# Optimization experiments

Measured on AMD Instinct MI355X. Metric: run time of the kernel, lower is better.

Reference implementation:

```python
import jax, jax.numpy as jnp
import numpy as np


def setup_inputs() -> dict:
    key = jax.random.key(0)
    k1, k2 = jax.random.split(key)
    x = jax.random.normal(k1, (128, 25, 512), dtype=jnp.float32)
    high = jax.random.normal(k2, (64, 20, 512), dtype=jnp.float32)  # (C, n, d)
    return {"x": x, "high": high}


def reference(x, high):
    # x: (b, res, d); high: (C, n, d) learned per-class support basis
    b, res, d = x.shape
    C, n, _ = high.shape
    q = x.reshape(b * res, d)                     # (Q, d)
    lam = n / d                                   # ridge coefficient = n/d
    ct = jnp.swapaxes(high, 1, 2)                 # (C, d, n)
    cct = high @ ct                               # (C, n, n) small Gram matrices
    inv = jnp.linalg.inv(cct + lam * jnp.eye(n, dtype=x.dtype))  # (C, n, n)
    ctinv = ct @ inv @ high                       # (C, d, d) per-class projector
    # reconstruct each query through each class projector: (C, Q, d)
    t = jnp.einsum('qd,cde->cqe', q, ctinv)
    dist = jnp.sum((t - q[None, :, :]) ** 2, axis=2).T  # (Q, C)
    logits = -dist.reshape(b, res, C).mean(axis=1)       # (b, C)
    # min-max scaler per row
    mn = logits.min(axis=1, keepdims=True)
    mx = logits.max(axis=1, keepdims=True)
    return (logits - mn) / (mx - mn)
```

## Files before the change

kernel.cpp:

```cpp
#include <hip/hip_runtime.h>

typedef __bf16 v8bf __attribute__((ext_vector_type(8)));
typedef float  v4f  __attribute__((ext_vector_type(4)));

#define D     512
#define NSUP  20
#define NC    64
#define RES   25
#define BB    128
#define LAM   (20.0f/512.0f)
#define KT    32
#define NKT   (D/KT)
#define CPB   8
#define COLS  160
#define NFRAG 10
#define MFRAG 4
#define LRSZ  820

__device__ __forceinline__ ushort bf_hi(float v) {
    uint32_t b = __float_as_uint(v);
    return (ushort)((b + 0x7FFF + ((b >> 16) & 1)) >> 16);
}
__device__ __forceinline__ float us2f(ushort u) {
    return __uint_as_float(((uint32_t)u) << 16);
}

__global__ __launch_bounds__(256) void k_prep1(const float* __restrict__ high,
                                               float* __restrict__ LR) {
    const int cls = blockIdx.x;
    const int t   = threadIdx.x;
    __shared__ float Hc[NSUP * 516];
    __shared__ float Gs[NSUP * NSUP];

    for (int i = t; i < NSUP * (D / 4); i += 256) {
        int r = i >> 7, c4 = (i & 127) << 2;
        *(float4*)&Hc[r * 516 + c4] = *(const float4*)&high[(cls * NSUP + r) * D + c4];
    }
    __syncthreads();

    for (int e = t; e < NSUP * NSUP; e += 256) {
        int i = e / NSUP, j = e % NSUP;
        if (i <= j) {
            float s = 0.f;
            for (int k = 0; k < D; k += 4) {
                float4 a = *(float4*)&Hc[i * 516 + k];
                float4 b = *(float4*)&Hc[j * 516 + k];
                s += a.x * b.x + a.y * b.y + a.z * b.z + a.w * b.w;
            }
            Gs[i * NSUP + j] = s;
            Gs[j * NSUP + i] = s;
        }
    }
    __syncthreads();

    if (t < 64) {
        const int c  = t & 31;
        const int gp = t >> 5;
        const float dlam = gp ? 2.0f * LAM : LAM;
        float m[NSUP];
        if (c < NSUP) {
            #pragma unroll
            for (int i = 0; i < NSUP; ++i) m[i] = Gs[i * NSUP + c];
            #pragma unroll
            for (int i = 0; i < NSUP; ++i) if (i == c) m[i] += dlam;
        }
        #pragma unroll
        for (int k = 0; k < NSUP; ++k) {
            float piv = __shfl(m[k], k, 32);
            float sq  = sqrtf(piv);
            float rsq = 1.0f / sq;
            float lck = m[k] * rsq;
            if (c == k) {
                m[k] = sq;
                #pragma unroll
                for (int i = k + 1; i < NSUP; ++i) m[i] *= rsq;
            }
            #pragma unroll
            for (int i = k + 1; i < NSUP; ++i) {
                float lik = __shfl(m[i], k, 32);
                if (c > k) m[i] -= lik * lck;
            }
        }
        if (c < NSUP) {
            float* base = LR + cls * LRSZ + (gp ? 400 : 0);
            #pragma unroll
            for (int i = 0; i < NSUP; ++i) if (i >= c) base[i * NSUP + c] = m[i];
            if (!gp) LR[cls * LRSZ + 800 + c] = 1.0f / m[c];
        }
    }
}

__global__ __launch_bounds__(256) void k_prep2(const float* __restrict__ high,
                                               const float* __restrict__ LR,
                                               ushort* __restrict__ Hth,
                                               ushort* __restrict__ Htl) {
    const int cls = blockIdx.x;
    const int col = blockIdx.y * 256 + threadIdx.x;
    const int t   = threadIdx.x;
    __shared__ float Ls[400], Rs[400], rL[NSUP];

    for (int i = t; i < 400; i += 256) Ls[i] = LR[cls * LRSZ + i];
    for (int i = t; i < 400; i += 256) Rs[i] = LR[cls * LRSZ + 400 + i];
    if (t < NSUP) rL[t] = LR[cls * LRSZ + 800 + t];
    __syncthreads();

    float h[NSUP];
    #pragma unroll
    for (int m = 0; m < NSUP; ++m) h[m] = high[(cls * NSUP + m) * D + col];
    #pragma unroll
    for (int i = 0; i < NSUP; ++i) {
        float s = h[i];
        #pragma unroll
        for (int m = 0; m < i; ++m) s -= Ls[i * NSUP + m] * h[m];
        h[i] = s * rL[i];
    }
    #pragma unroll
    for (int i = NSUP - 1; i >= 0; --i) {
        float s = h[i];
        #pragma unroll
        for (int m = i + 1; m < NSUP; ++m) s -= Ls[m * NSUP + i] * h[m];
        h[i] = s * rL[i];
    }
    #pragma unroll
    for (int i = 0; i < NSUP; ++i) {
        float s = 0.f;
        #pragma unroll
        for (int m = i; m < NSUP; ++m) s += Rs[m * NSUP + i] * h[m];
        ushort hh = bf_hi(s);
        float  rr = s - us2f(hh);
        Hth[(cls * NSUP + i) * D + col] = hh;
        Htl[(cls * NSUP + i) * D + col] = bf_hi(rr);
    }
}

__global__ __launch_bounds__(256, 2) void k_main(const float* __restrict__ x,
                                                 const ushort* __restrict__ Hth,
                                                 const ushort* __restrict__ Htl,
                                                 float* __restrict__ S) {
    const int cg = blockIdx.x, bp = blockIdx.y;
    const int t = threadIdx.x, lane = t & 63, wid = t >> 6;
    const int wm = wid >> 1, wn = wid & 1;

    __shared__ __align__(16) ushort XH[2][MFRAG * 512];
    __shared__ __align__(16) ushort XL[2][MFRAG * 512];
    __shared__ __align__(16) ushort HH[2][NFRAG * 512];
    __shared__ __align__(16) ushort HL[2][NFRAG * 512];
    __shared__ float colsum[2][COLS];

    v4f acc[2][5];
    #pragma unroll
    for (int a = 0; a < 2; ++a)
        #pragma unroll
        for (int b = 0; b < 5; ++b) acc[a][b] = (v4f){0.f, 0.f, 0.f, 0.f};

    auto stageX = [&](int buf, int kt) {
        #pragma unroll
        for (int s2 = 0; s2 < 2; ++s2) {
            int g = t + 256 * s2;
            int p = g >> 3;
            int k0 = (g & 7) << 2;
            float4 v = make_float4(0.f, 0.f, 0.f, 0.f);
            int r = p & 31;
            if (r < RES)
                v = *(const float4*)&x[(((bp << 1) + (p >> 5)) * RES + r) * D + kt + k0];
            ushort4 hu, lu;
            {
                ushort h; float rr;
                h = bf_hi(v.x); rr = v.x - us2f(h); hu.x = h; lu.x = bf_hi(rr);
                h = bf_hi(v.y); rr = v.y - us2f(h); hu.y = h; lu.y = bf_hi(rr);
                h = bf_hi(v.z); rr = v.z - us2f(h); hu.z = h; lu.z = bf_hi(rr);
                h = bf_hi(v.w); rr = v.w - us2f(h); hu.w = h; lu.w = bf_hi(rr);
            }
            int m = p >> 4, i = p & 15, q = k0 >> 3, off = (k0 & 7);
            int base = m * 512 + (q * 16 + i) * 8 + off;
            *(ushort4*)&XH[buf][base] = hu;
            *(ushort4*)&XL[buf][base] = lu;
        }
    };

    auto stageH = [&](int buf, int kt) {
        #pragma unroll
        for (int j = 0; j < 5; ++j) {
            int cid = wid * 5 + j;
            int n = (cid < 10) ? cid : cid - 10;
            const ushort* src = (cid < 10) ? Hth : Htl;
            ushort* dst = (cid < 10) ? &HH[buf][n * 512] : &HL[buf][n * 512];
            int row = cg * COLS + n * 16 + (lane & 15);
            const ushort* gp = &src[row * D + kt + ((lane >> 4) << 3)];
            __builtin_amdgcn_global_load_lds(
                (const __attribute__((address_space(1))) void*)gp,
                (__attribute__((address_space(3))) void*)dst, 16, 0, 0);
        }
    };

    auto compute = [&](int buf) {
        v8bf ah[2], al[2];
        #pragma unroll
        for (int mf = 0; mf < 2; ++mf) {
            int f = wm * 2 + mf;
            ah[mf] = *(const v8bf*)&XH[buf][f * 512 + lane * 8];
            al[mf] = *(const v8bf*)&XL[buf][f * 512 + lane * 8];
        }
        #pragma unroll
        for (int nf = 0; nf < 5; ++nf) {
            int f = wn * 5 + nf;
            v8bf bh = *(const v8bf*)&HH[buf][f * 512 + lane * 8];
            v8bf bl = *(const v8bf*)&HL[buf][f * 512 + lane * 8];
            #pragma unroll
            for (int mf = 0; mf < 2; ++mf) {
                acc[mf][nf] = __builtin_amdgcn_mfma_f32_16x16x32_bf16(ah[mf], bh, acc[mf][nf], 0, 0, 0);
                acc[mf][nf] = __builtin_amdgcn_mfma_f32_16x16x32_bf16(ah[mf], bl, acc[mf][nf], 0, 0, 0);
                acc[mf][nf] = __builtin_amdgcn_mfma_f32_16x16x32_bf16(al[mf], bh, acc[mf][nf], 0, 0, 0);
            }
        }
    };

    stageX(0, 0);
    stageH(0, 0);
    __syncthreads();
    for (int step = 0; step < NKT; ++step) {
        int cur = step & 1;
        if (step + 1 < NKT) {
            stageH(cur ^ 1, (step + 1) * KT);
            stageX(cur ^ 1, (step + 1) * KT);
        }
        compute(cur);
        __syncthreads();
    }

    #pragma unroll
    for (int nf = 0; nf < 5; ++nf) {
        float part = 0.f;
        #pragma unroll
        for (int mf = 0; mf < 2; ++mf)
            #pragma unroll
            for (int j = 0; j < 4; ++j) part += acc[mf][nf][j] * acc[mf][nf][j];
        part += __shfl_xor(part, 16);
        part += __shfl_xor(part, 32);
        if ((lane >> 4) == 0) colsum[wm][wn * 80 + nf * 16 + lane] = part;
    }
    __syncthreads();
    if (t < 16) {
        int b = t >> 3, c = t & 7;
        float s = 0.f;
        #pragma unroll
        for (int i = 0; i < NSUP; ++i) s += colsum[b][c * 20 + i];
        S[((bp << 1) + b) * NC + cg * CPB + c] = s;
    }
}

__global__ __launch_bounds__(64) void k_minmax(const float* __restrict__ S,
                                               float* __restrict__ out) {
    const int b    = blockIdx.x;
    const int lane = threadIdx.x;
    float s  = S[b * NC + lane];
    float mn = s, mx = s;
    #pragma unroll
    for (int off = 32; off > 0; off >>= 1) {
        mn = fminf(mn, __shfl_xor(mn, off, 64));
        mx = fmaxf(mx, __shfl_xor(mx, off, 64));
    }
    out[b * NC + lane] = (s - mn) / (mx - mn);
}

extern "C" void kernel_launch(void* const* d_in, const int* in_sizes, int n_in,
                              void* d_out, int out_size, void* d_ws, size_t ws_size,
                              hipStream_t stream) {
    const float* x    = (const float*)d_in[0];
    const float* high = (const float*)d_in[1];
    float* out = (float*)d_out;

    ushort* Hth = (ushort*)d_ws;
    ushort* Htl = Hth + NC * NSUP * D;
    float*  S   = (float*)(Htl + NC * NSUP * D);
    float*  LR  = S + BB * NC;

    k_prep1 <<<NC, 256, 0, stream>>>(high, LR);
    k_prep2 <<<dim3(NC, 2), 256, 0, stream>>>(high, LR, Hth, Htl);
    k_main  <<<dim3(CPB, BB / 2), 256, 0, stream>>>(x, Hth, Htl, S);
    k_minmax<<<BB, 64, 0, stream>>>(S, out);
}
```

Before: 110.9 us.

## Fuse prep kernels and fold min-max normalization into main kernel via tickets

Merges the two preparation kernels into one, so each block computes the Cholesky factors in shared memory and applies them directly instead of round-tripping through global memory. Each of the two blocks per class recomputes the Gram and factorization redundantly. The final min-max kernel is removed: the last main-kernel block for each batch pair, found with an atomic ticket counter, normalizes the rows. This cuts two kernel launches and adds atomics and fences.

```diff
diff --git a/kernel.cpp b/kernel.cpp
--- a/kernel.cpp
+++ b/kernel.cpp
@@ -15,7 +15,6 @@
 #define COLS  160
 #define NFRAG 10
 #define MFRAG 4
-#define LRSZ  820
 
 __device__ __forceinline__ ushort bf_hi(float v) {
     uint32_t b = __float_as_uint(v);
@@ -25,12 +24,18 @@
     return __uint_as_float(((uint32_t)u) << 16);
 }
 
-__global__ __launch_bounds__(256) void k_prep1(const float* __restrict__ high,
-                                               float* __restrict__ LR) {
-    const int cls = blockIdx.x;
-    const int t   = threadIdx.x;
+__global__ __launch_bounds__(256) void k_prep(const float* __restrict__ high,
+                                              ushort* __restrict__ Hth,
+                                              ushort* __restrict__ Htl,
+                                              int* __restrict__ ticket) {
+    const int cls  = blockIdx.x;
+    const int half = blockIdx.y;
+    const int t    = threadIdx.x;
     __shared__ float Hc[NSUP * 516];
     __shared__ float Gs[NSUP * NSUP];
+    __shared__ float Ls[400], Rs[400], rL[NSUP];
+
+    if (cls == 0 && half == 0 && t < NC) ticket[t] = 0;
 
     for (int i = t; i < NSUP * (D / 4); i += 256) {
         int r = i >> 7, c4 = (i & 127) << 2;
@@ -82,31 +87,18 @@
             }
         }
         if (c < NSUP) {
-            float* base = LR + cls * LRSZ + (gp ? 400 : 0);
-            #pragma unroll
-            for (int i = 0; i < NSUP; ++i) if (i >= c) base[i * NSUP + c] = m[i];
-            if (!gp) LR[cls * LRSZ + 800 + c] = 1.0f / m[c];
-        }
-    }
-}
-
-__global__ __launch_bounds__(256) void k_prep2(const float* __restrict__ high,
-                                               const float* __restrict__ LR,
-                                               ushort* __restrict__ Hth,
-                                               ushort* __restrict__ Htl) {
-    const int cls = blockIdx.x;
-    const int col = blockIdx.y * 256 + threadIdx.x;
-    const int t   = threadIdx.x;
-    __shared__ float Ls[400], Rs[400], rL[NSUP];
-
-    for (int i = t; i < 400; i += 256) Ls[i] = LR[cls * LRSZ + i];
-    for (int i = t; i < 400; i += 256) Rs[i] = LR[cls * LRSZ + 400 + i];
-    if (t < NSUP) rL[t] = LR[cls * LRSZ + 800 + t];
-    __syncthreads();
-
+            float* Lout = gp ? Rs : Ls;
+            #pragma unroll
+            for (int i = 0; i < NSUP; ++i) if (i >= c) Lout[i * NSUP + c] = m[i];
+            if (!gp) rL[c] = 1.0f / m[c];
+        }
+    }
+    __syncthreads();
+
+    const int col = half * 256 + t;
     float h[NSUP];
     #pragma unroll
-    for (int m = 0; m < NSUP; ++m) h[m] = high[(cls * NSUP + m) * D + col];
+    for (int m = 0; m < NSUP; ++m) h[m] = Hc[m * 516 + col];
     #pragma unroll
     for (int i = 0; i < NSUP; ++i) {
         float s = h[i];
@@ -136,7 +128,9 @@
 __global__ __launch_bounds__(256, 2) void k_main(const float* __restrict__ x,
                                                  const ushort* __restrict__ Hth,
                                                  const ushort* __restrict__ Htl,
-                                                 float* __restrict__ S) {
+                                                 float* __restrict__ S,
+                                                 int* __restrict__ ticket,
+                                                 float* __restrict__ out) {
     const int cg = blockIdx.x, bp = blockIdx.y;
     const int t = threadIdx.x, lane = t & 63, wid = t >> 6;
     const int wm = wid >> 1, wn = wid & 1;
@@ -146,6 +140,7 @@
     __shared__ __align__(16) ushort HH[2][NFRAG * 512];
     __shared__ __align__(16) ushort HL[2][NFRAG * 512];
     __shared__ float colsum[2][COLS];
+    __shared__ int lastflag;
 
     v4f acc[2][5];
     #pragma unroll
@@ -245,22 +240,29 @@
         float s = 0.f;
         #pragma unroll
         for (int i = 0; i < NSUP; ++i) s += colsum[b][c * 20 + i];
-        S[((bp << 1) + b) * NC + cg * CPB + c] = s;
-    }
-}
-
-__global__ __launch_bounds__(64) void k_minmax(const float* __restrict__ S,
-                                               float* __restrict__ out) {
-    const int b    = blockIdx.x;
-    const int lane = threadIdx.x;
-    float s  = S[b * NC + lane];
-    float mn = s, mx = s;
-    #pragma unroll
-    for (int off = 32; off > 0; off >>= 1) {
-        mn = fminf(mn, __shfl_xor(mn, off, 64));
-        mx = fmaxf(mx, __shfl_xor(mx, off, 64));
-    }
-    out[b * NC + lane] = (s - mn) / (mx - mn);
+        __hip_atomic_store(&S[((bp << 1) + b) * NC + cg * CPB + c], s,
+                           __ATOMIC_RELAXED, __HIP_MEMORY_SCOPE_AGENT);
+    }
+    __syncthreads();
+    __threadfence();
+    if (t == 0) {
+        int old = atomicAdd(&ticket[bp], 1);
+        lastflag = (old == CPB - 1);
+    }
+    __syncthreads();
+    if (lastflag && t < 128) {
+        int row = (bp << 1) + (t >> 6);
+        int c   = t & 63;
+        float s = __hip_atomic_load(&S[row * NC + c],
+                                    __ATOMIC_RELAXED, __HIP_MEMORY_SCOPE_AGENT);
+        float mn = s, mx = s;
+        #pragma unroll
+        for (int off = 32; off > 0; off >>= 1) {
+            mn = fminf(mn, __shfl_xor(mn, off, 64));
+            mx = fmaxf(mx, __shfl_xor(mx, off, 64));
+        }
+        out[row * NC + c] = (s - mn) / (mx - mn);
+    }
 }
 
 extern "C" void kernel_launch(void* const* d_in, const int* in_sizes, int n_in,
@@ -270,13 +272,11 @@
     const float* high = (const float*)d_in[1];
     float* out = (float*)d_out;
 
-    ushort* Hth = (ushort*)d_ws;
-    ushort* Htl = Hth + NC * NSUP * D;
-    float*  S   = (float*)(Htl + NC * NSUP * D);
-    float*  LR  = S + BB * NC;
-
-    k_prep1 <<<NC, 256, 0, stream>>>(high, LR);
-    k_prep2 <<<dim3(NC, 2), 256, 0, stream>>>(high, LR, Hth, Htl);
-    k_main  <<<dim3(CPB, BB / 2), 256, 0, stream>>>(x, Hth, Htl, S);
-    k_minmax<<<BB, 64, 0, stream>>>(S, out);
-}
+    ushort* Hth    = (ushort*)d_ws;
+    ushort* Htl    = Hth + NC * NSUP * D;
+    float*  S      = (float*)(Htl + NC * NSUP * D);
+    int*    ticket = (int*)(S + BB * NC);
+
+    k_prep <<<dim3(NC, 2), 256, 0, stream>>>(high, Hth, Htl, ticket);
+    k_main <<<dim3(CPB, BB / 2), 256, 0, stream>>>(x, Hth, Htl, S, ticket, out);
+}
```

Result: slower. 135.0 us (+21.7%).

## Fuse prep kernels and load MFMA operands directly from global memory

Applied to the files above, without the earlier changes.

Merges the two prep kernels into one per-(class, half) block that computes the Cholesky factors in shared memory and solves directly, removing one launch and the LR round trip through global memory. The Gram/Cholesky work is now duplicated across the two halves. The main kernel drops its LDS double-buffered staging and syncthreads, loading x and the projected basis straight from global into MFMA fragments, and raises occupancy to 4 blocks per CU. The risk is exposed global-load latency with no software pipelining, plus redundant x conversion and loads across waves.

```diff
diff --git a/kernel.cpp b/kernel.cpp
--- a/kernel.cpp
+++ b/kernel.cpp
@@ -13,9 +13,6 @@
 #define NKT   (D/KT)
 #define CPB   8
 #define COLS  160
-#define NFRAG 10
-#define MFRAG 4
-#define LRSZ  820
 
 __device__ __forceinline__ ushort bf_hi(float v) {
     uint32_t b = __float_as_uint(v);
@@ -25,12 +22,15 @@
     return __uint_as_float(((uint32_t)u) << 16);
 }
 
-__global__ __launch_bounds__(256) void k_prep1(const float* __restrict__ high,
-                                               float* __restrict__ LR) {
-    const int cls = blockIdx.x;
-    const int t   = threadIdx.x;
+__global__ __launch_bounds__(256) void k_prep(const float* __restrict__ high,
+                                              ushort* __restrict__ Hth,
+                                              ushort* __restrict__ Htl) {
+    const int cls  = blockIdx.x;
+    const int half = blockIdx.y;
+    const int t    = threadIdx.x;
     __shared__ float Hc[NSUP * 516];
     __shared__ float Gs[NSUP * NSUP];
+    __shared__ float Ls[400], Rs[400], rL[NSUP];
 
     for (int i = t; i < NSUP * (D / 4); i += 256) {
         int r = i >> 7, c4 = (i & 127) << 2;
@@ -82,31 +82,18 @@
             }
         }
         if (c < NSUP) {
-            float* base = LR + cls * LRSZ + (gp ? 400 : 0);
-            #pragma unroll
-            for (int i = 0; i < NSUP; ++i) if (i >= c) base[i * NSUP + c] = m[i];
-            if (!gp) LR[cls * LRSZ + 800 + c] = 1.0f / m[c];
-        }
-    }
-}
-
-__global__ __launch_bounds__(256) void k_prep2(const float* __restrict__ high,
-                                               const float* __restrict__ LR,
-                                               ushort* __restrict__ Hth,
-                                               ushort* __restrict__ Htl) {
-    const int cls = blockIdx.x;
-    const int col = blockIdx.y * 256 + threadIdx.x;
-    const int t   = threadIdx.x;
-    __shared__ float Ls[400], Rs[400], rL[NSUP];
-
-    for (int i = t; i < 400; i += 256) Ls[i] = LR[cls * LRSZ + i];
-    for (int i = t; i < 400; i += 256) Rs[i] = LR[cls * LRSZ + 400 + i];
-    if (t < NSUP) rL[t] = LR[cls * LRSZ + 800 + t];
-    __syncthreads();
-
+            float* Lout = gp ? Rs : Ls;
+            #pragma unroll
+            for (int i = 0; i < NSUP; ++i) if (i >= c) Lout[i * NSUP + c] = m[i];
+            if (!gp) rL[c] = 1.0f / m[c];
+        }
+    }
+    __syncthreads();
+
+    const int col = half * 256 + t;
     float h[NSUP];
     #pragma unroll
-    for (int m = 0; m < NSUP; ++m) h[m] = high[(cls * NSUP + m) * D + col];
+    for (int m = 0; m < NSUP; ++m) h[m] = Hc[m * 516 + col];
     #pragma unroll
     for (int i = 0; i < NSUP; ++i) {
         float s = h[i];
@@ -133,18 +120,15 @@
     }
 }
 
-__global__ __launch_bounds__(256, 2) void k_main(const float* __restrict__ x,
+__global__ __launch_bounds__(256, 4) void k_main(const float* __restrict__ x,
                                                  const ushort* __restrict__ Hth,
                                                  const ushort* __restrict__ Htl,
                                                  float* __restrict__ S) {
     const int cg = blockIdx.x, bp = blockIdx.y;
     const int t = threadIdx.x, lane = t & 63, wid = t >> 6;
     const int wm = wid >> 1, wn = wid & 1;
-
-    __shared__ __align__(16) ushort XH[2][MFRAG * 512];
-    __shared__ __align__(16) ushort XL[2][MFRAG * 512];
-    __shared__ __align__(16) ushort HH[2][NFRAG * 512];
-    __shared__ __align__(16) ushort HL[2][NFRAG * 512];
+    const int r16 = lane & 15, q = lane >> 4;
+
     __shared__ float colsum[2][COLS];
 
     v4f acc[2][5];
@@ -153,59 +137,49 @@
         #pragma unroll
         for (int b = 0; b < 5; ++b) acc[a][b] = (v4f){0.f, 0.f, 0.f, 0.f};
 
-    auto stageX = [&](int buf, int kt) {
-        #pragma unroll
-        for (int s2 = 0; s2 < 2; ++s2) {
-            int g = t + 256 * s2;
-            int p = g >> 3;
-            int k0 = (g & 7) << 2;
-            float4 v = make_float4(0.f, 0.f, 0.f, 0.f);
-            int r = p & 31;
-            if (r < RES)
-                v = *(const float4*)&x[(((bp << 1) + (p >> 5)) * RES + r) * D + kt + k0];
-            ushort4 hu, lu;
-            {
-                ushort h; float rr;
-                h = bf_hi(v.x); rr = v.x - us2f(h); hu.x = h; lu.x = bf_hi(rr);
-                h = bf_hi(v.y); rr = v.y - us2f(h); hu.y = h; lu.y = bf_hi(rr);
-                h = bf_hi(v.z); rr = v.z - us2f(h); hu.z = h; lu.z = bf_hi(rr);
-                h = bf_hi(v.w); rr = v.w - us2f(h); hu.w = h; lu.w = bf_hi(rr);
-            }
-            int m = p >> 4, i = p & 15, q = k0 >> 3, off = (k0 & 7);
-            int base = m * 512 + (q * 16 + i) * 8 + off;
-            *(ushort4*)&XH[buf][base] = hu;
-            *(ushort4*)&XL[buf][base] = lu;
-        }
-    };
-
-    auto stageH = [&](int buf, int kt) {
-        #pragma unroll
-        for (int j = 0; j < 5; ++j) {
-            int cid = wid * 5 + j;
-            int n = (cid < 10) ? cid : cid - 10;
-            const ushort* src = (cid < 10) ? Hth : Htl;
-            ushort* dst = (cid < 10) ? &HH[buf][n * 512] : &HL[buf][n * 512];
-            int row = cg * COLS + n * 16 + (lane & 15);
-            const ushort* gp = &src[row * D + kt + ((lane >> 4) << 3)];
-            __builtin_amdgcn_global_load_lds(
-                (const __attribute__((address_space(1))) void*)gp,
-                (__attribute__((address_space(3))) void*)dst, 16, 0, 0);
-        }
-    };
-
-    auto compute = [&](int buf) {
+    bool  avalid[2];
+    const float* aptr[2];
+    #pragma unroll
+    for (int mf = 0; mf < 2; ++mf) {
+        int f  = wm * 2 + mf;
+        int tr = f * 16 + r16;
+        int batch = (bp << 1) + (tr >> 5);
+        int rb = tr & 31;
+        avalid[mf] = rb < RES;
+        aptr[mf] = &x[(batch * RES + (avalid[mf] ? rb : 0)) * D + (q << 3)];
+    }
+    const ushort* bptrh[5];
+    const ushort* bptrl[5];
+    #pragma unroll
+    for (int nf = 0; nf < 5; ++nf) {
+        int f   = wn * 5 + nf;
+        int row = cg * COLS + f * 16 + r16;
+        bptrh[nf] = &Hth[row * D + (q << 3)];
+        bptrl[nf] = &Htl[row * D + (q << 3)];
+    }
+
+    for (int kt = 0; kt < D; kt += KT) {
         v8bf ah[2], al[2];
         #pragma unroll
         for (int mf = 0; mf < 2; ++mf) {
-            int f = wm * 2 + mf;
-            ah[mf] = *(const v8bf*)&XH[buf][f * 512 + lane * 8];
-            al[mf] = *(const v8bf*)&XL[buf][f * 512 + lane * 8];
+            float4 v0 = make_float4(0.f, 0.f, 0.f, 0.f), v1 = v0;
+            if (avalid[mf]) {
+                v0 = *(const float4*)(aptr[mf] + kt);
+                v1 = *(const float4*)(aptr[mf] + kt + 4);
+            }
+            float vv[8] = {v0.x, v0.y, v0.z, v0.w, v1.x, v1.y, v1.z, v1.w};
+            #pragma unroll
+            for (int e = 0; e < 8; ++e) {
+                ushort h = bf_hi(vv[e]);
+                float  r = vv[e] - us2f(h);
+                ((ushort*)&ah[mf])[e] = h;
+                ((ushort*)&al[mf])[e] = bf_hi(r);
+            }
         }
         #pragma unroll
         for (int nf = 0; nf < 5; ++nf) {
-            int f = wn * 5 + nf;
-            v8bf bh = *(const v8bf*)&HH[buf][f * 512 + lane * 8];
-            v8bf bl = *(const v8bf*)&HL[buf][f * 512 + lane * 8];
+            v8bf bh = *(const v8bf*)(bptrh[nf] + kt);
+            v8bf bl = *(const v8bf*)(bptrl[nf] + kt);
             #pragma unroll
             for (int mf = 0; mf < 2; ++mf) {
                 acc[mf][nf] = __builtin_amdgcn_mfma_f32_16x16x32_bf16(ah[mf], bh, acc[mf][nf], 0, 0, 0);
@@ -213,19 +187,6 @@
                 acc[mf][nf] = __builtin_amdgcn_mfma_f32_16x16x32_bf16(al[mf], bh, acc[mf][nf], 0, 0, 0);
             }
         }
-    };
-
-    stageX(0, 0);
-    stageH(0, 0);
-    __syncthreads();
-    for (int step = 0; step < NKT; ++step) {
-        int cur = step & 1;
-        if (step + 1 < NKT) {
-            stageH(cur ^ 1, (step + 1) * KT);
-            stageX(cur ^ 1, (step + 1) * KT);
-        }
-        compute(cur);
-        __syncthreads();
     }
 
     #pragma unroll
@@ -237,7 +198,7 @@
             for (int j = 0; j < 4; ++j) part += acc[mf][nf][j] * acc[mf][nf][j];
         part += __shfl_xor(part, 16);
         part += __shfl_xor(part, 32);
-        if ((lane >> 4) == 0) colsum[wm][wn * 80 + nf * 16 + lane] = part;
+        if (q == 0) colsum[wm][wn * 80 + nf * 16 + r16] = part;
     }
     __syncthreads();
     if (t < 16) {
@@ -273,10 +234,8 @@
     ushort* Hth = (ushort*)d_ws;
     ushort* Htl = Hth + NC * NSUP * D;
     float*  S   = (float*)(Htl + NC * NSUP * D);
-    float*  LR  = S + BB * NC;
-
-    k_prep1 <<<NC, 256, 0, stream>>>(high, LR);
-    k_prep2 <<<dim3(NC, 2), 256, 0, stream>>>(high, LR, Hth, Htl);
+
+    k_prep  <<<dim3(NC, 2), 256, 0, stream>>>(high, Hth, Htl);
     k_main  <<<dim3(CPB, BB / 2), 256, 0, stream>>>(x, Hth, Htl, S);
     k_minmax<<<BB, 64, 0, stream>>>(S, out);
 }
```

Result: slower. 124.5 us (+12.3%).
